# Kernel optimization log

Hardware: AMD Instinct MI355X
Metric: run time of the kernel (lower is better)

## Reference

```python
import jax, jax.numpy as jnp
import numpy as np

B, T, C, H = 4, 2048, 1024, 16
D = C // H


def setup_inputs() -> dict:
    key = jax.random.key(0)
    ks = jax.random.split(key, 5)
    s = 0.02
    return {
        "x": jax.random.normal(ks[0], (B, T, C), dtype=jnp.float32),
        "W_attn": jax.random.normal(ks[1], (C, 3 * C), dtype=jnp.float32) * s,
        "b_attn": jax.random.normal(ks[2], (3 * C,), dtype=jnp.float32) * s,
        "W_proj": jax.random.normal(ks[3], (C, C), dtype=jnp.float32) * s,
        "b_proj": jax.random.normal(ks[4], (C,), dtype=jnp.float32) * s,
    }


def reference(x, W_attn, b_attn, W_proj, b_proj):
    # QKV projection: [B,T,3C]
    qkv = x @ W_attn + b_attn
    q, k, v = jnp.split(qkv, 3, axis=-1)
    # [B,T,C] -> [B,H,T,D]
    def to_heads(t):
        return t.reshape(B, T, H, D).transpose(0, 2, 1, 3)
    q, k, v = to_heads(q), to_heads(k), to_heads(v)
    scale = 1.0 / np.sqrt(D).astype(np.float32)
    # full (non-causal) attention scores [B,H,T,T]
    att = jnp.einsum("bhqd,bhkd->bhqk", q, k) * scale
    att = jax.nn.softmax(att, axis=-1)
    y = jnp.einsum("bhqk,bhkd->bhqd", att, v)
    y = y.transpose(0, 2, 1, 3).reshape(B, T, C)
    return y @ W_proj + b_proj
```

## Files before the change

### kernel.cpp

```cpp
#include <hip/hip_runtime.h>

#define BATCH 4
#define SEQ   2048
#define CDIM  1024
#define NHEAD 16
#define HDIM  64
#define BH    (BATCH * NHEAD)
#define MROWS (BATCH * SEQ)

typedef __attribute__((ext_vector_type(8))) short  short8;
typedef __attribute__((ext_vector_type(4))) float  floatx4;

#define MFMA_BF16(a, b, c) __builtin_amdgcn_mfma_f32_16x16x32_bf16((a), (b), (c), 0, 0, 0)

#define GLOAD16(g, l) __builtin_amdgcn_global_load_lds( \
    (__attribute__((address_space(1))) void*)(g),       \
    (__attribute__((address_space(3))) void*)(l), 16, 0, 0)

__device__ __forceinline__ unsigned short f2bf(float f) {
    union { float f; unsigned u; } v; v.f = f;
    unsigned u = v.u;
    return (unsigned short)((u + 0x7FFFu + ((u >> 16) & 1u)) >> 16);
}

__device__ __forceinline__ float fast_exp2(float x) {
#if __has_builtin(__builtin_amdgcn_exp2f)
    return __builtin_amdgcn_exp2f(x);
#else
    return exp2f(x);
#endif
}

__device__ __forceinline__ unsigned pack_bf16_trunc(float a, float b) {
    union { float f; unsigned u; } ua, ub;
    ua.f = a; ub.f = b;
    return __builtin_amdgcn_perm(ub.u, ua.u, 0x07060302u);
}

__global__ __launch_bounds__(256) void conv_bf16_kernel(
    const float* __restrict__ in, unsigned short* __restrict__ out)
{
    int i = (blockIdx.x * 256 + threadIdx.x) * 4;
    float4 v = *(const float4*)(in + i);
    ushort4 o;
    o.x = f2bf(v.x); o.y = f2bf(v.y); o.z = f2bf(v.z); o.w = f2bf(v.w);
    *(ushort4*)(out + i) = o;
}

__global__ __launch_bounds__(256) void conv_wt_kernel(
    const float* __restrict__ in, unsigned short* __restrict__ out, int K, int N)
{
    __shared__ float T[64][68];
    const int k0 = blockIdx.y * 64, n0 = blockIdx.x * 64;
    const int tid = threadIdx.x;
    const int r = tid >> 4, c4 = (tid & 15) * 4;
    #pragma unroll
    for (int i = 0; i < 4; ++i) {
        int row = r + i * 16;
        float4 v = *(const float4*)(in + (size_t)(k0 + row) * N + n0 + c4);
        T[row][c4 + 0] = v.x; T[row][c4 + 1] = v.y;
        T[row][c4 + 2] = v.z; T[row][c4 + 3] = v.w;
    }
    __syncthreads();
    #pragma unroll
    for (int i = 0; i < 4; ++i) {
        int nrow = r + i * 16;
        ushort4 o;
        o.x = f2bf(T[c4 + 0][nrow]); o.y = f2bf(T[c4 + 1][nrow]);
        o.z = f2bf(T[c4 + 2][nrow]); o.w = f2bf(T[c4 + 3][nrow]);
        *(ushort4*)(out + (size_t)(n0 + nrow) * K + k0 + c4) = o;
    }
}

__global__ __launch_bounds__(256) void qkv_mfma_kernel(
    const unsigned short* __restrict__ A,
    const unsigned short* __restrict__ Bt,
    const float* __restrict__ bias,
    unsigned short* __restrict__ Qo,
    unsigned short* __restrict__ Ko,
    unsigned short* __restrict__ Vo)
{
    const int K = CDIM;
    __shared__ __align__(16) unsigned short As[128 * 32];
    __shared__ __align__(16) unsigned short Bs[128 * 32];

    const int tid = threadIdx.x;
    const int m0 = blockIdx.y * 128, n0 = blockIdx.x * 128;
    const int w = tid >> 6, lane = tid & 63;
    const int wm = (w >> 1) * 64, wn = (w & 1) * 64;
    const int lm = lane & 15, kg = lane >> 4;

    floatx4 acc[4][4];
    const floatx4 zf = {0.f, 0.f, 0.f, 0.f};
    #pragma unroll
    for (int mt = 0; mt < 4; ++mt)
        #pragma unroll
        for (int nt = 0; nt < 4; ++nt) acc[mt][nt] = zf;

    #pragma unroll 1
    for (int k0 = 0; k0 < K; k0 += 32) {
        __syncthreads();
        #pragma unroll
        for (int i = 0; i < 2; ++i) {
            int ci = i * 256 + tid;
            GLOAD16(A  + (size_t)(m0 + (ci >> 2)) * K + k0 + (ci & 3) * 8, As + ci * 8);
            GLOAD16(Bt + (size_t)(n0 + (ci >> 2)) * K + k0 + (ci & 3) * 8, Bs + ci * 8);
        }
        __syncthreads();
        short8 af[4], bf[4];
        #pragma unroll
        for (int t = 0; t < 4; ++t) {
            af[t] = *(const short8*)(As + (wm + t * 16 + lm) * 32 + kg * 8);
            bf[t] = *(const short8*)(Bs + (wn + t * 16 + lm) * 32 + kg * 8);
        }
        #pragma unroll
        for (int mt = 0; mt < 4; ++mt)
            #pragma unroll
            for (int nt = 0; nt < 4; ++nt)
                acc[mt][nt] = MFMA_BF16(af[mt], bf[nt], acc[mt][nt]);
    }

    #pragma unroll
    for (int nt = 0; nt < 4; ++nt) {
        int col = n0 + wn + nt * 16 + lm;
        float bv = bias[col];
        int which = col >> 10;
        int c1 = col & 1023;
        int h = c1 >> 6, d = c1 & 63;
        #pragma unroll
        for (int mt = 0; mt < 4; ++mt) {
            int mbase = m0 + wm + mt * 16 + kg * 4;
            int b = mbase >> 11;
            int t = mbase & 2047;
            int bh = b * NHEAD + h;
            if (which == 2) {
                ushort4 o;
                o.x = f2bf(acc[mt][nt][0] + bv);
                o.y = f2bf(acc[mt][nt][1] + bv);
                o.z = f2bf(acc[mt][nt][2] + bv);
                o.w = f2bf(acc[mt][nt][3] + bv);
                *(ushort4*)(Vo + ((size_t)bh * 64 + d) * SEQ + t) = o;
            } else {
                unsigned short* dst = (which == 0) ? Qo : Ko;
                float qs = (which == 0) ? 0.18033688011112042f : 1.0f;
                #pragma unroll
                for (int r = 0; r < 4; ++r)
                    dst[((size_t)bh * SEQ + t + r) * 64 + d] =
                        f2bf((acc[mt][nt][r] + bv) * qs);
            }
        }
    }
}

__global__ __launch_bounds__(256) void proj_mfma_kernel(
    const unsigned short* __restrict__ A,
    const unsigned short* __restrict__ Bt,
    const float* __restrict__ bias,
    float* __restrict__ out)
{
    const int K = CDIM;
    __shared__ __align__(16) unsigned short As[128 * 32];
    __shared__ __align__(16) unsigned short Bs[128 * 32];

    const int tid = threadIdx.x;
    const int m0 = blockIdx.y * 128, n0 = blockIdx.x * 128;
    const int w = tid >> 6, lane = tid & 63;
    const int wm = (w >> 1) * 64, wn = (w & 1) * 64;
    const int lm = lane & 15, kg = lane >> 4;

    floatx4 acc[4][4];
    const floatx4 zf = {0.f, 0.f, 0.f, 0.f};
    #pragma unroll
    for (int mt = 0; mt < 4; ++mt)
        #pragma unroll
        for (int nt = 0; nt < 4; ++nt) acc[mt][nt] = zf;

    #pragma unroll 1
    for (int k0 = 0; k0 < K; k0 += 32) {
        __syncthreads();
        #pragma unroll
        for (int i = 0; i < 2; ++i) {
            int ci = i * 256 + tid;
            GLOAD16(A  + (size_t)(m0 + (ci >> 2)) * K + k0 + (ci & 3) * 8, As + ci * 8);
            GLOAD16(Bt + (size_t)(n0 + (ci >> 2)) * K + k0 + (ci & 3) * 8, Bs + ci * 8);
        }
        __syncthreads();
        short8 af[4], bf[4];
        #pragma unroll
        for (int t = 0; t < 4; ++t) {
            af[t] = *(const short8*)(As + (wm + t * 16 + lm) * 32 + kg * 8);
            bf[t] = *(const short8*)(Bs + (wn + t * 16 + lm) * 32 + kg * 8);
        }
        #pragma unroll
        for (int mt = 0; mt < 4; ++mt)
            #pragma unroll
            for (int nt = 0; nt < 4; ++nt)
                acc[mt][nt] = MFMA_BF16(af[mt], bf[nt], acc[mt][nt]);
    }

    #pragma unroll
    for (int nt = 0; nt < 4; ++nt) {
        int col = n0 + wn + nt * 16 + lm;
        float bv = bias[col];
        #pragma unroll
        for (int mt = 0; mt < 4; ++mt) {
            int mbase = m0 + wm + mt * 16 + kg * 4;
            #pragma unroll
            for (int r = 0; r < 4; ++r)
                out[(size_t)(mbase + r) * CDIM + col] = acc[mt][nt][r] + bv;
        }
    }
}

#define BUFSH 8192

__device__ __forceinline__ void attn_stage_tile(
    const unsigned short* __restrict__ Kg,
    const unsigned short* __restrict__ Vg,
    size_t base, int kb, unsigned short* buf, int tid)
{
    unsigned short* Kb_ = buf;
    unsigned short* Vb_ = buf + 4096;
    #pragma unroll
    for (int i = 0; i < 2; ++i) {
        int lin = i * 256 + tid;
        int srow = lin >> 3;
        int chunk = lin & 7;
        int s2 = srow & 31;
        int grow = (srow & 32) + ((s2 >> 2) & 3) * 8 + ((s2 >> 4) & 1) * 4 + (s2 & 3);
        int gch = chunk ^ (srow & 7);
        GLOAD16(Kg + base + (size_t)(kb * 64 + grow) * 64 + gch * 8, Kb_ + lin * 8);
        GLOAD16(Vg + base + (size_t)srow * SEQ + kb * 64 + gch * 8, Vb_ + lin * 8);
    }
}

__global__ __launch_bounds__(256) void attn_mfma_kernel(
    const unsigned short* __restrict__ Qg,
    const unsigned short* __restrict__ Kg,
    const unsigned short* __restrict__ Vg,
    unsigned short* __restrict__ Y)
{
    __shared__ __align__(16) unsigned short Smem[2 * BUFSH];

    const int tid = threadIdx.x, w = tid >> 6, lane = tid & 63;
    const int lm = lane & 15, kg = lane >> 4;
    const int qb = blockIdx.x, bh = blockIdx.y;
    const size_t base = (size_t)bh * SEQ * 64;

    short8 qf[4][2];
    #pragma unroll
    for (int nt = 0; nt < 4; ++nt)
        #pragma unroll
        for (int c = 0; c < 2; ++c)
            qf[nt][c] = *(const short8*)(
                Qg + base + (size_t)(qb * 256 + w * 64 + nt * 16 + lm) * 64 + c * 32 + kg * 8);

    const floatx4 zf = {0.f, 0.f, 0.f, 0.f};
    floatx4 O[4][4];
    #pragma unroll
    for (int nt = 0; nt < 4; ++nt)
        #pragma unroll
        for (int nd = 0; nd < 4; ++nd) O[nt][nd] = zf;
    float lsum[4] = {0.f, 0.f, 0.f, 0.f};

    attn_stage_tile(Kg, Vg, base, 0, Smem, tid);

    #pragma unroll 1
    for (int kb = 0; kb < SEQ / 64; ++kb) {
        __syncthreads();
        if (kb + 1 < SEQ / 64)
            attn_stage_tile(Kg, Vg, base, kb + 1, Smem + ((kb + 1) & 1) * BUFSH, tid);

        const unsigned short* Ksb = Smem + (kb & 1) * BUFSH;
        const unsigned short* Vsb = Ksb + 4096;
        const int sw = (lm & 7);

        #pragma unroll
        for (int ch = 0; ch < 2; ++ch) {
            uint4 pa[4];
            #pragma unroll
            for (int mt = 0; mt < 2; ++mt) {
                floatx4 st[4];
                #pragma unroll
                for (int nt = 0; nt < 4; ++nt) st[nt] = zf;
                #pragma unroll
                for (int c = 0; c < 2; ++c) {
                    short8 kf = *(const short8*)(
                        Ksb + (ch * 32 + mt * 16 + lm) * 64 + ((c * 4 + kg) ^ sw) * 8);
                    #pragma unroll
                    for (int nt = 0; nt < 4; ++nt)
                        st[nt] = MFMA_BF16(kf, qf[nt][c], st[nt]);
                }
                #pragma unroll
                for (int nt = 0; nt < 4; ++nt) {
                    float e0 = fast_exp2(st[nt][0]);
                    float e1 = fast_exp2(st[nt][1]);
                    float e2 = fast_exp2(st[nt][2]);
                    float e3 = fast_exp2(st[nt][3]);
                    lsum[nt] += (e0 + e1) + (e2 + e3);
                    if (mt == 0) {
                        pa[nt].x = pack_bf16_trunc(e0, e1);
                        pa[nt].y = pack_bf16_trunc(e2, e3);
                    } else {
                        pa[nt].z = pack_bf16_trunc(e0, e1);
                        pa[nt].w = pack_bf16_trunc(e2, e3);
                    }
                }
            }
            #pragma unroll
            for (int nd = 0; nd < 4; ++nd) {
                short8 vb = *(const short8*)(
                    Vsb + (nd * 16 + lm) * 64 + ((ch * 4 + kg) ^ sw) * 8);
                #pragma unroll
                for (int nt = 0; nt < 4; ++nt) {
                    short8 paf;
                    __builtin_memcpy(&paf, &pa[nt], 16);
                    O[nt][nd] = MFMA_BF16(paf, vb, O[nt][nd]);
                }
            }
        }
    }

    #pragma unroll
    for (int nt = 0; nt < 4; ++nt) {
        lsum[nt] += __shfl_xor(lsum[nt], 16);
        lsum[nt] += __shfl_xor(lsum[nt], 32);
    }
    float linv[4][4];
    #pragma unroll
    for (int mq = 0; mq < 4; ++mq)
        #pragma unroll
        for (int r = 0; r < 4; ++r)
            linv[mq][r] = 1.0f / __shfl(lsum[mq], kg * 4 + r);

    const int b = bh >> 4, h = bh & 15;
    #pragma unroll
    for (int mq = 0; mq < 4; ++mq)
        #pragma unroll
        for (int r = 0; r < 4; ++r) {
            int t = qb * 256 + w * 64 + mq * 16 + kg * 4 + r;
            #pragma unroll
            for (int nd = 0; nd < 4; ++nd)
                Y[((size_t)(b * SEQ + t)) * CDIM + h * 64 + nd * 16 + lm] =
                    f2bf(O[mq][nd][r] * linv[mq][r]);
        }
}

extern "C" void kernel_launch(void* const* d_in, const int* in_sizes, int n_in,
                              void* d_out, int out_size, void* d_ws, size_t ws_size,
                              hipStream_t stream) {
    const float* x      = (const float*)d_in[0];
    const float* W_attn = (const float*)d_in[1];
    const float* b_attn = (const float*)d_in[2];
    const float* W_proj = (const float*)d_in[3];
    const float* b_proj = (const float*)d_in[4];
    float* out = (float*)d_out;

    char* ws = (char*)d_ws;
    unsigned short* xb  = (unsigned short*)(ws);
    unsigned short* Wat = (unsigned short*)(ws + (size_t)16777216);
    unsigned short* Wpt = (unsigned short*)(ws + (size_t)23068672);
    unsigned short* Qb  = (unsigned short*)(ws + (size_t)25165824);
    unsigned short* Kb  = (unsigned short*)(ws + (size_t)41943040);
    unsigned short* Vtb = (unsigned short*)(ws + (size_t)58720256);
    unsigned short* Yb  = (unsigned short*)(ws + (size_t)75497472);

    conv_bf16_kernel<<<dim3(MROWS * CDIM / 1024), 256, 0, stream>>>(x, xb);
    conv_wt_kernel<<<dim3(3 * CDIM / 64, CDIM / 64), 256, 0, stream>>>(
        W_attn, Wat, CDIM, 3 * CDIM);
    conv_wt_kernel<<<dim3(CDIM / 64, CDIM / 64), 256, 0, stream>>>(
        W_proj, Wpt, CDIM, CDIM);

    qkv_mfma_kernel<<<dim3(3 * CDIM / 128, MROWS / 128), 256, 0, stream>>>(
        xb, Wat, b_attn, Qb, Kb, Vtb);

    attn_mfma_kernel<<<dim3(SEQ / 256, BH), 256, 0, stream>>>(Qb, Kb, Vtb, Yb);

    proj_mfma_kernel<<<dim3(CDIM / 128, MROWS / 128), 256, 0, stream>>>(
        Yb, Wpt, b_proj, out);
}
```

Measured before the change: 294.3 us.

## Double-buffer LDS tiles in QKV and projection GEMM kernels

Both MFMA GEMM kernels now use two LDS buffers per operand. The next K-slice is prefetched with global_load_lds into the alternate buffer while the current slice is being computed. This removes one of the two barriers per K-step and hides global load latency behind MFMA work. The cost is double the LDS footprint per block (32 KB), which may lower occupancy. Correctness relies on the barrier waiting for the outstanding async loads.

New measurement: 283.2 us. 1.04x faster.

```diff
diff --git a/kernel.cpp b/kernel.cpp
--- a/kernel.cpp
+++ b/kernel.cpp
@@ -72,6 +72,20 @@
     }
 }
 
+#define GBUF (128 * 32)
+
+__device__ __forceinline__ void gemm_stage(
+    const unsigned short* __restrict__ A, const unsigned short* __restrict__ Bt,
+    int K, int m0, int n0, int k0, unsigned short* As, unsigned short* Bs, int tid)
+{
+    #pragma unroll
+    for (int i = 0; i < 2; ++i) {
+        int ci = i * 256 + tid;
+        GLOAD16(A  + (size_t)(m0 + (ci >> 2)) * K + k0 + (ci & 3) * 8, As + ci * 8);
+        GLOAD16(Bt + (size_t)(n0 + (ci >> 2)) * K + k0 + (ci & 3) * 8, Bs + ci * 8);
+    }
+}
+
 __global__ __launch_bounds__(256) void qkv_mfma_kernel(
     const unsigned short* __restrict__ A,
     const unsigned short* __restrict__ Bt,
@@ -81,8 +95,8 @@
     unsigned short* __restrict__ Vo)
 {
     const int K = CDIM;
-    __shared__ __align__(16) unsigned short As[128 * 32];
-    __shared__ __align__(16) unsigned short Bs[128 * 32];
+    __shared__ __align__(16) unsigned short As2[2 * GBUF];
+    __shared__ __align__(16) unsigned short Bs2[2 * GBUF];
 
     const int tid = threadIdx.x;
     const int m0 = blockIdx.y * 128, n0 = blockIdx.x * 128;
@@ -97,16 +111,16 @@
         #pragma unroll
         for (int nt = 0; nt < 4; ++nt) acc[mt][nt] = zf;
 
+    gemm_stage(A, Bt, K, m0, n0, 0, As2, Bs2, tid);
+
     #pragma unroll 1
-    for (int k0 = 0; k0 < K; k0 += 32) {
+    for (int kt = 0; kt < K / 32; ++kt) {
         __syncthreads();
-        #pragma unroll
-        for (int i = 0; i < 2; ++i) {
-            int ci = i * 256 + tid;
-            GLOAD16(A  + (size_t)(m0 + (ci >> 2)) * K + k0 + (ci & 3) * 8, As + ci * 8);
-            GLOAD16(Bt + (size_t)(n0 + (ci >> 2)) * K + k0 + (ci & 3) * 8, Bs + ci * 8);
-        }
-        __syncthreads();
+        if (kt + 1 < K / 32)
+            gemm_stage(A, Bt, K, m0, n0, (kt + 1) * 32,
+                       As2 + ((kt + 1) & 1) * GBUF, Bs2 + ((kt + 1) & 1) * GBUF, tid);
+        const unsigned short* As = As2 + (kt & 1) * GBUF;
+        const unsigned short* Bs = Bs2 + (kt & 1) * GBUF;
         short8 af[4], bf[4];
         #pragma unroll
         for (int t = 0; t < 4; ++t) {
@@ -159,8 +173,8 @@
     float* __restrict__ out)
 {
     const int K = CDIM;
-    __shared__ __align__(16) unsigned short As[128 * 32];
-    __shared__ __align__(16) unsigned short Bs[128 * 32];
+    __shared__ __align__(16) unsigned short As2[2 * GBUF];
+    __shared__ __align__(16) unsigned short Bs2[2 * GBUF];
 
     const int tid = threadIdx.x;
     const int m0 = blockIdx.y * 128, n0 = blockIdx.x * 128;
@@ -175,16 +189,16 @@
         #pragma unroll
         for (int nt = 0; nt < 4; ++nt) acc[mt][nt] = zf;
 
+    gemm_stage(A, Bt, K, m0, n0, 0, As2, Bs2, tid);
+
     #pragma unroll 1
-    for (int k0 = 0; k0 < K; k0 += 32) {
+    for (int kt = 0; kt < K / 32; ++kt) {
         __syncthreads();
-        #pragma unroll
-        for (int i = 0; i < 2; ++i) {
-            int ci = i * 256 + tid;
-            GLOAD16(A  + (size_t)(m0 + (ci >> 2)) * K + k0 + (ci & 3) * 8, As + ci * 8);
-            GLOAD16(Bt + (size_t)(n0 + (ci >> 2)) * K + k0 + (ci & 3) * 8, Bs + ci * 8);
-        }
-        __syncthreads();
+        if (kt + 1 < K / 32)
+            gemm_stage(A, Bt, K, m0, n0, (kt + 1) * 32,
+                       As2 + ((kt + 1) & 1) * GBUF, Bs2 + ((kt + 1) & 1) * GBUF, tid);
+        const unsigned short* As = As2 + (kt & 1) * GBUF;
+        const unsigned short* Bs = Bs2 + (kt & 1) * GBUF;
         short8 af[4], bf[4];
         #pragma unroll
         for (int t = 0; t < 4; ++t) {
```
